# Optimization experiments

Hardware: AMD Instinct MI355X
Metric: run time of the kernel (lower is better)

Reference implementation:

```python
import math
import jax, jax.numpy as jnp
import numpy as np

# h_data constants (init_kwargs)
PITCH = 0.0003      # [m]
FS = 40000000.0     # [Hz]
TX_ANGLE = 0.1      # [rad]
C = 1540.0          # [m/s]
T0 = 0.0            # [s]
CLIP = -70.0        # [dB]
EPS = np.float32(np.finfo(np.float32).eps)


def interplin(v, ds, sq):
    """Vectorized per-column linear interpolation: v(sq[:,k], k).
    v: (N, K) float, sq: (N, K) query points in physical units, ds: step size.
    """
    n = v.shape[0]
    iq = sq / ds
    oob = ~(iq < n - 2)
    iqc = jnp.where(oob, 0.0, iq)
    fl = jnp.floor(iqc).astype(jnp.int32)
    lw = iqc - fl
    v0 = jnp.take_along_axis(v, fl, axis=0)
    v1 = jnp.take_along_axis(v, fl + 1, axis=0)
    vq = v0 * (1.0 - lw) + v1 * lw
    return jnp.where(oob, 0.0, vq)


def fkmig(data):
    """Stolt f-k migration for one (nt, nx) plane-wave RF frame."""
    nt, nx = data.shape
    nt_shift = 2 * math.ceil(T0 * FS / 2)
    nt_fft = 4 * nt + nt_shift              # 8192
    nx_fft = 2 * math.ceil(4 * nx / 2)      # 512
    nf = nt_fft // 2 + 1                    # 4097

    f_vec = jnp.arange(nf, dtype=jnp.float32) * (FS / nt_fft)          # (nf,)
    kx_vec = jnp.roll(jnp.arange(-nx_fft // 2, nx_fft // 2, dtype=jnp.float32) + 1,
                      nx_fft // 2 + 1) / PITCH / nx_fft                # (nx_fft,)
    f = f_vec[:, None]    # (nf, 1)
    kx = kx_vec[None, :]  # (1, nx_fft)

    ol = jnp.fft.fft(data, nt_fft, axis=0)[:nf, :]                     # (nf, nx) complex

    sin_a = math.sin(TX_ANGLE)
    cos_a = math.cos(TX_ANGLE)
    t_delay = sin_a * ((nx - 1) * int(TX_ANGLE < 0)
                       - jnp.arange(nx, dtype=jnp.float32)) * (PITCH / C)  # (nx,)
    ol = ol * jnp.exp(-2j * math.pi * (t_delay + T0)[None, :] * f).astype(jnp.complex64)
    ol = jnp.fft.fft(ol, nx_fft, axis=1)                               # (nf, nx_fft)

    v_erm = C / math.sqrt(1 + cos_a + sin_a ** 2)
    beta = (1 + cos_a) ** 1.5 / (1 + cos_a + sin_a ** 2)
    kz = 2 * f / (beta * C)
    f_kz = v_erm * jnp.sqrt(kx ** 2 + kz ** 2)                         # (nf, nx_fft)

    evanescent = (jnp.abs(f) / (jnp.abs(kx) + EPS)) < C
    ol = jnp.where(evanescent, 0, ol)

    ds = FS / nt_fft
    ol = interplin(ol.real, ds, f_kz) + 1j * interplin(ol.imag, ds, f_kz)
    ol = ol * (f / (f_kz + EPS))
    ol = ol.at[0].set(0)

    # hermitian extension of the half spectrum
    oln = jnp.conj(jnp.fliplr(jnp.roll(ol, -1, axis=1)))
    inv_idx = jnp.arange(nt_fft // 2 - 1, 0, -1)
    ol = jnp.concatenate([ol, oln[inv_idx]], axis=0)                   # (nt_fft, nx_fft)
    ol = jnp.fft.ifft(ol, axis=0)

    gamma = sin_a / (2 - cos_a)
    dx = -gamma * (jnp.arange(nt_fft, dtype=jnp.float32) / FS) * C / 2
    ol = ol * jnp.exp(-2j * math.pi * kx_vec[None, :] * dx[:, None]).astype(jnp.complex64)
    ol = jnp.fft.ifft(ol, axis=1)
    return ol[nt_shift:nt_shift + nt, :nx]                             # (nt, nx) complex


def image_formation(mig):
    """Envelope detection (hilbert along axis 0) + log compression on (nt, nx) real."""
    nt = mig.shape[0]
    Xf = jnp.fft.fft(mig, nt, axis=0)
    h = np.zeros(nt, np.float32)
    if nt % 2 == 0:
        h[0] = h[nt // 2] = 1
        h[1:nt // 2] = 2
    else:
        h[0] = 1
        h[1:(nt + 1) // 2] = 2
    analytic = jnp.fft.ifft(Xf * jnp.asarray(h)[:, None], axis=0)
    img = 20.0 * jnp.log10(jnp.abs(analytic))
    img = img - jnp.max(img)
    img = jnp.where(img < CLIP, CLIP, img)
    return (img + abs(CLIP)) / abs(CLIP)


def setup_inputs() -> dict:
    key = jax.random.key(0)
    data = jax.random.normal(key, (4, 2048, 128), dtype=jnp.float32)
    return {"data": data}


def reference(data):
    mig = jax.vmap(fkmig)(data)                 # (B, nt, nx) complex
    img = jax.vmap(image_formation)(jnp.real(mig))
    return img
```

## Files before the change

kernel.cpp:

```cpp
#include <hip/hip_runtime.h>
#include <cmath>

#define NT 2048
#define NX 128
#define NXF 512
#define NF 4097
#define NFP 4104
#define TDP 2056
#define NBATCH 4
#define EPSF 1.1920929e-07f
#define SOUND_C 1540.0f
#define TWO_PI 6.283185307179586f

__device__ __forceinline__ int SK(int e) { return e + 2 * (e >> 4); }

struct FKP {
  float ds, inv_ds, inv_kx_den, v_erm, kz_coef, ph_rev, dx_coef;
};

__device__ __forceinline__ float2 cmul(float2 a, float2 b) {
  return make_float2(a.x * b.x - a.y * b.y, a.x * b.y + a.y * b.x);
}
__device__ __forceinline__ float2 twid(float u) {
  const float a = u * TWO_PI;
  return make_float2(__cosf(a), __sinf(a));
}
__device__ __forceinline__ float2 twidf(float u) {
  u -= floorf(u);
  return twid(u);
}
__device__ __forceinline__ int dr4_3(unsigned m) {
  unsigned r = __brev(m) >> 26;
  return (int)(((r & 0x15u) << 1) | ((r >> 1) & 0x15u));
}
__device__ __forceinline__ int dr4_4(unsigned m) {
  unsigned r = __brev(m) >> 24;
  return (int)(((r & 0x55u) << 1) | ((r >> 1) & 0x55u));
}
__device__ __forceinline__ int dr4_5(unsigned m) {
  unsigned r = __brev(m) >> 22;
  return (int)(((r & 0x155u) << 1) | ((r >> 1) & 0x155u));
}

__device__ __forceinline__ void dft4(float2& A, float2& B, float2& C, float2& D, float sgn) {
  float2 t0 = make_float2(A.x + C.x, A.y + C.y);
  float2 t1 = make_float2(A.x - C.x, A.y - C.y);
  float2 t2 = make_float2(B.x + D.x, B.y + D.y);
  float2 t3 = make_float2(B.x - D.x, B.y - D.y);
  float2 r  = make_float2(-sgn * t3.y, sgn * t3.x);
  A = make_float2(t0.x + t2.x, t0.y + t2.y);
  B = make_float2(t1.x + r.x, t1.y + r.y);
  C = make_float2(t0.x - t2.x, t0.y - t2.y);
  D = make_float2(t1.x - r.x, t1.y - r.y);
}
__device__ __forceinline__ void bfly4r(float2& A, float2& B, float2& C, float2& D,
                                       float2 w1, float2 w2, float2 w3, float sgn) {
  B = cmul(B, w1); C = cmul(C, w2); D = cmul(D, w3);
  dft4(A, B, C, D, sgn);
}
__device__ __forceinline__ void twtrip(float u, float2& w1, float2& w2, float2& w3) {
  w1 = twid(u); w2 = cmul(w1, w1); w3 = cmul(w2, w1);
}

template<int S>
__device__ __forceinline__ void mstage(float2* __restrict__ s, int base, int kb, float sgn) {
  float2 w[16];
#pragma unroll
  for (int m = 0; m < 16; ++m) w[m] = s[SK(base + S * m)];
  {
    float2 a1, a2, a3; twtrip(sgn * (float)kb * (1.0f / (4 * S)), a1, a2, a3);
#pragma unroll
    for (int a = 0; a < 4; ++a)
      bfly4r(w[4 * a], w[4 * a + 1], w[4 * a + 2], w[4 * a + 3], a1, a2, a3, sgn);
  }
#pragma unroll
  for (int c = 0; c < 4; ++c) {
    float2 b1, b2, b3; twtrip(sgn * (float)(kb + S * c) * (1.0f / (16 * S)), b1, b2, b3);
    bfly4r(w[c], w[4 + c], w[8 + c], w[12 + c], b1, b2, b3, sgn);
  }
#pragma unroll
  for (int m = 0; m < 16; ++m) s[SK(base + S * m)] = w[m];
}

__global__ void __launch_bounds__(256) k_tr(const float* __restrict__ data,
                                            float* __restrict__ dt,
                                            float* __restrict__ red,
                                            size_t slot4, int b_base) {
  __shared__ float tile[32][33];
  if (threadIdx.x == 0 && blockIdx.x == 0 && blockIdx.y == 0)
    *(unsigned*)&red[blockIdx.z * slot4] = 0u;
  const int tx = threadIdx.x & 31;
  const int ty = threadIdx.x >> 5;
  const int t0 = blockIdx.x * 32;
  const int x0 = blockIdx.y * 32;
  const float* In = data + (size_t)(b_base + blockIdx.z) * NT * NX;
  float* Dt = dt + blockIdx.z * slot4;
  for (int i = ty; i < 32; i += 8)
    tile[i][tx] = In[(size_t)(t0 + i) * NX + x0 + tx];
  __syncthreads();
  for (int i = ty; i < 32; i += 8)
    Dt[(size_t)(x0 + i) * TDP + t0 + tx] = tile[tx][i];
}

__global__ void __launch_bounds__(256) k_fft_t(const float* __restrict__ dt,
                                               float2* __restrict__ o1t,
                                               size_t slot4, size_t slot8, FKP P) {
  __shared__ float2 nat[1152];
  __shared__ float2 s[4608];
  const int x = blockIdx.x, tid = threadIdx.x;
  const float2* row2 = (const float2*)(dt + blockIdx.z * slot4 + (size_t)x * TDP);
  float2* O1 = o1t + blockIdx.z * slot8 + (size_t)x * NFP;
  for (int m = tid; m < 1024; m += 256) nat[SK(m)] = row2[m];
  __syncthreads();
  {
    const int m0 = dr4_4((unsigned)tid);
    const float2 v0 = nat[SK(m0)];
    const float2 v1 = nat[SK(m0 + 256)];
    const float2 v2 = nat[SK(m0 + 512)];
    const float2 v3 = nat[SK(m0 + 768)];
    const int base = tid << 4;
#pragma unroll
    for (int k = 0; k < 4; ++k) {
      float2 A = v0, B = v1, C = v2, D = v3;
      if (k == 0) {
        dft4(A, B, C, D, -1.0f);
      } else {
        float2 w1, w2, w3; twtrip(-(float)k * (1.0f / 16.0f), w1, w2, w3);
        bfly4r(A, B, C, D, w1, w2, w3, -1.0f);
      }
      s[SK(base + k)] = A; s[SK(base + 4 + k)] = B;
      s[SK(base + 8 + k)] = C; s[SK(base + 12 + k)] = D;
    }
  }
  __syncthreads();
  mstage<16>(s, ((tid >> 4) << 8) | (tid & 15), tid & 15, -1.0f);
  __syncthreads();
  mstage<256>(s, tid, tid, -1.0f);
  __syncthreads();
  for (int k = tid; k < NF; k += 256) {
    const int ka = k & 4095, kb = (4096 - k) & 4095;
    const float2 Ck = s[SK(ka)];
    const float2 Cm = s[SK(kb)];
    float2 E = make_float2(0.5f * (Ck.x + Cm.x), 0.5f * (Ck.y - Cm.y));
    float2 T = make_float2(0.5f * (Ck.x - Cm.x), 0.5f * (Ck.y + Cm.y));
    float2 WT = cmul(twid((float)k * (-1.0f / 8192.0f)), T);
    float2 X = make_float2(E.x + WT.y, E.y - WT.x);
    float2 ph = twidf(P.ph_rev * (float)(x * k));
    O1[k] = cmul(X, ph);
  }
}

#define R2P 580
__global__ void __launch_bounds__(512) k_fft_x(const float2* __restrict__ o1t,
                                               float2* __restrict__ ot,
                                               size_t slot8, FKP P) {
  __shared__ float2 s[8 * R2P];
  const int i0 = blockIdx.x * 8;
  const int tid = threadIdx.x;
  const float2* O1 = o1t + blockIdx.z * slot8;
  float2* OT = ot + blockIdx.z * slot8;
  for (int idx = tid; idx < 128 * 8; idx += 512) {
    const int ii = idx & 7, x = idx >> 3;
    const int i = i0 + ii;
    float2 v = (i < NF) ? O1[(size_t)x * NFP + i] : make_float2(0.f, 0.f);
    float2* r = s + ii * R2P;
    const int p = ((x & 1) << 8) + 4 * dr4_3((unsigned)(x >> 1));
    r[SK(p)] = v; r[SK(p + 1)] = v; r[SK(p + 2)] = v; r[SK(p + 3)] = v;
  }
  __syncthreads();
  for (int mh = 4; mh <= 64; mh *= 4) {
    const float inv = -1.0f / (float)(4 * mh);
    for (int t = tid; t < 8 * 128; t += 512) {
      const int row = t >> 7, tt = t & 127;
      const int half = tt >> 6, q = tt & 63;
      const int k = q & (mh - 1);
      const int i0b = ((q & ~(mh - 1)) << 2) + k + (half << 8);
      float2* r = s + row * R2P;
      float2 A = r[SK(i0b)], B = r[SK(i0b + mh)], C = r[SK(i0b + 2 * mh)], D = r[SK(i0b + 3 * mh)];
      float2 w1, w2, w3; twtrip((float)k * inv, w1, w2, w3);
      bfly4r(A, B, C, D, w1, w2, w3, -1.0f);
      r[SK(i0b)] = A; r[SK(i0b + mh)] = B; r[SK(i0b + 2 * mh)] = C; r[SK(i0b + 3 * mh)] = D;
    }
    __syncthreads();
  }
  for (int t = tid; t < 8 * 256; t += 512) {
    const int row = t >> 8, k = t & 255;
    float2* r = s + row * R2P;
    float2 E = r[SK(k)], O = r[SK(256 + k)];
    float2 WO = cmul(twid((float)k * (-1.0f / 512.0f)), O);
    r[SK(k)]       = make_float2(E.x + WO.x, E.y + WO.y);
    r[SK(256 + k)] = make_float2(E.x - WO.x, E.y - WO.y);
  }
  __syncthreads();
  for (int idx = tid; idx < 512 * 8; idx += 512) {
    const int j = idx >> 3, ii = idx & 7;
    const int i = i0 + ii;
    if (i >= NF) continue;
    const float f = P.ds * (float)i;
    const int kn = (j <= 256) ? j : j - 512;
    const float kx = fabsf((float)kn * P.inv_kx_den);
    float2 v = (f / (kx + EPSF) < SOUND_C) ? make_float2(0.f, 0.f)
                                           : s[ii * R2P + SK(j)];
    OT[(size_t)j * NFP + i] = v;
  }
}

__global__ void __launch_bounds__(512) k_ifft_t(const float2* __restrict__ ot,
                                                float2* __restrict__ tdt,
                                                size_t slot8, FKP P) {
  __shared__ float2 s[9216];
  const int j = blockIdx.x;
  const int jm = (NXF - j) & (NXF - 1);
  const int t = threadIdx.x;
  const float2* OT = ot + blockIdx.z * slot8;
  float2* T = tdt + blockIdx.z * slot8 + (size_t)j * TDP;
  const float kxj = (float)j * P.inv_kx_den;
  const float kx2 = kxj * kxj;
  const float2* rowj = OT + (size_t)j * NFP;
  const float2* rowm = OT + (size_t)jm * NFP;
  {
    const int tau = t & 255, half = t >> 8;
    const int m0 = dr4_4((unsigned)tau);
    float2 w[16];
#pragma unroll
    for (int m = 0; m < 16; ++m) {
      const int ci = (m & 3) * 1024 + (m >> 2) * 256 + m0;
      const int n = 2 * ci + half;
      const bool mir = (n > 4096);
      const int r = mir ? (8192 - n) : n;
      const float2* rw = mir ? rowm : rowj;
      float2 v = make_float2(0.f, 0.f);
      if (r > 0) {
        const float f = P.ds * (float)r;
        const float kz = f * P.kz_coef;
        const float fkz = P.v_erm * sqrtf(kx2 + kz * kz);
        const float iq = fkz * P.inv_ds;
        if (iq < 4095.0f) {
          const float flf = floorf(iq);
          const int fl = (int)flf;
          const float lw = iq - flf;
          const float2 v0 = rw[fl], v1 = rw[fl + 1];
          const float sc = f / (fkz + EPSF);
          v.x = (v0.x + (v1.x - v0.x) * lw) * sc;
          v.y = (v0.y + (v1.y - v0.y) * lw) * (mir ? -sc : sc);
        }
      }
      w[m] = v;
    }
#pragma unroll
    for (int a = 0; a < 4; ++a) dft4(w[4 * a], w[4 * a + 1], w[4 * a + 2], w[4 * a + 3], 1.0f);
    dft4(w[0], w[4], w[8], w[12], 1.0f);
#pragma unroll
    for (int k = 1; k < 4; ++k) {
      float2 w1, w2, w3; twtrip((float)k * (1.0f / 16.0f), w1, w2, w3);
      bfly4r(w[k], w[4 + k], w[8 + k], w[12 + k], w1, w2, w3, 1.0f);
    }
    const int base = t << 4;
#pragma unroll
    for (int m = 0; m < 16; ++m) s[SK(base + m)] = w[m];
  }
  __syncthreads();
  mstage<16>(s, ((t >> 4) << 8) | (t & 15), t & 15, 1.0f);
  __syncthreads();
  mstage<256>(s, ((t >> 8) << 12) | (t & 255), t & 255, 1.0f);
  __syncthreads();
  const float dxr = -kxj * P.dx_coef;
#pragma unroll
  for (int i = 0; i < 4; ++i) {
    const int k = t + 512 * i;
    const float2 E = s[SK(k)];
    const float2 O = s[SK(4096 + k)];
    const float2 WO = cmul(twid((float)k * (1.0f / 8192.0f)), O);
    const float2 y = make_float2(E.x + WO.x, E.y + WO.y);
    T[k] = cmul(y, twidf(dxr * (float)k));
  }
}

#define SXA 260
#define SXC 292
__global__ void __launch_bounds__(256) k_c2r_x(const float2* __restrict__ tdt,
                                               float* __restrict__ migt,
                                               size_t slot8, size_t slot4) {
  __shared__ float2 sx[8 * SXA];
  __shared__ float2 sc[8 * SXC];
  const int t0 = blockIdx.x * 8;
  const int tid = threadIdx.x;
  const float2* T = tdt + blockIdx.z * slot8;
  float* M = migt + blockIdx.z * slot4;
  for (int idx = tid; idx < 257 * 8; idx += 256) {
    const int tt = idx & 7, jj = idx >> 3;
    float2 v = T[(size_t)jj * TDP + t0 + tt];
    if (jj == 0 || jj == 256) v.y = 0.0f;
    sx[tt * SXA + jj] = v;
  }
  __syncthreads();
  for (int idx = tid; idx < 129 * 8; idx += 256) {
    const int row = idx & 7, k = idx >> 3;
    const float2* X = sx + row * SXA;
    float2* Cb = sc + row * SXC;
    const float2 Xk = X[k];
    const float2 Xm = X[256 - k];
    float2 Ef = make_float2(0.5f * (Xk.x + Xm.x), 0.5f * (Xk.y - Xm.y));
    float2 Tm = make_float2(0.5f * (Xk.x - Xm.x), 0.5f * (Xk.y + Xm.y));
    float2 Of = cmul(twid((float)k * (1.0f / 512.0f)), Tm);
    Cb[SK(dr4_4((unsigned)k))] = make_float2(Ef.x - Of.y, Ef.y + Of.x);
    if (k > 0 && k < 128)
      Cb[SK(dr4_4((unsigned)(256 - k)))] = make_float2(Ef.x + Of.y, Of.x - Ef.y);
  }
  __syncthreads();
  for (int mh = 1; mh <= 64; mh *= 4) {
    const float inv = 1.0f / (float)(4 * mh);
    for (int t = tid; t < 8 * 64; t += 256) {
      const int row = t >> 6, q = t & 63;
      const int k = q & (mh - 1);
      const int i0 = ((q & ~(mh - 1)) << 2) + k;
      float2* r = sc + row * SXC;
      float2 A = r[SK(i0)], B = r[SK(i0 + mh)], C = r[SK(i0 + 2 * mh)], D = r[SK(i0 + 3 * mh)];
      if (mh > 1) {
        float2 w1, w2, w3; twtrip((float)k * inv, w1, w2, w3);
        bfly4r(A, B, C, D, w1, w2, w3, 1.0f);
      } else {
        dft4(A, B, C, D, 1.0f);
      }
      r[SK(i0)] = A; r[SK(i0 + mh)] = B; r[SK(i0 + 2 * mh)] = C; r[SK(i0 + 3 * mh)] = D;
    }
    __syncthreads();
  }
  for (int idx = tid; idx < 128 * 8; idx += 256) {
    const int x = idx >> 3, tt = idx & 7;
    const float2 c = sc[tt * SXC + SK(x >> 1)];
    M[(size_t)x * TDP + t0 + tt] = (x & 1) ? c.y : c.x;
  }
}

__global__ void __launch_bounds__(512) k_hilbert(const float* __restrict__ migt,
                                                 float* __restrict__ migdb,
                                                 float* __restrict__ red,
                                                 size_t slot4) {
  __shared__ float2 s[2304];
  __shared__ float rmax[512];
  const int x = blockIdx.x, tid = threadIdx.x;
  const float* Mr = migt + blockIdx.z * slot4 + (size_t)x * TDP;
  float* Db = migdb + blockIdx.z * slot4 + (size_t)x * TDP;
#pragma unroll
  for (int i = 0; i < 4; ++i) {
    const int p = tid + 512 * i;
    s[SK(p)] = make_float2(Mr[p], 0.0f);
  }
  __syncthreads();
#pragma unroll
  for (int i = 0; i < 2; ++i) {
    const int p = tid + 512 * i;
    const float2 a = s[SK(p)], b = s[SK(p + 1024)];
    s[SK(p)] = make_float2(a.x + b.x, a.y + b.y);
    s[SK(p + 1024)] = cmul(make_float2(a.x - b.x, a.y - b.y),
                           twid(-(float)p * (1.0f / 2048.0f)));
  }
  __syncthreads();
  for (int mh = 256; mh >= 1; mh >>= 2) {
    const int half = tid >> 8, q = tid & 255;
    const int k = q & (mh - 1);
    const int i0 = (half << 10) + ((q & ~(mh - 1)) << 2) + k;
    float2 A = s[SK(i0)], B = s[SK(i0 + mh)], C = s[SK(i0 + 2 * mh)], D = s[SK(i0 + 3 * mh)];
    dft4(A, B, C, D, -1.0f);
    if (mh > 1) {
      float2 w1, w2, w3; twtrip(-(float)k / (float)(4 * mh), w1, w2, w3);
      B = cmul(B, w1); C = cmul(C, w2); D = cmul(D, w3);
    }
    s[SK(i0)] = A; s[SK(i0 + mh)] = B; s[SK(i0 + 2 * mh)] = C; s[SK(i0 + 3 * mh)] = D;
    __syncthreads();
  }
#pragma unroll
  for (int i = 0; i < 4; ++i) {
    const int p = tid + 512 * i;
    const int kk = 2 * dr4_5((unsigned)(p & 1023)) + (p >> 10);
    const float hv = (kk == 0 || kk == 1024) ? 1.0f : ((kk < 1024) ? 2.0f : 0.0f);
    float2 v = s[SK(p)];
    s[SK(p)] = make_float2(v.x * hv, v.y * hv);
  }
  __syncthreads();
  for (int mh = 1; mh <= 256; mh <<= 2) {
    const int half = tid >> 8, q = tid & 255;
    const int k = q & (mh - 1);
    const int i0 = (half << 10) + ((q & ~(mh - 1)) << 2) + k;
    float2 A = s[SK(i0)], B = s[SK(i0 + mh)], C = s[SK(i0 + 2 * mh)], D = s[SK(i0 + 3 * mh)];
    if (mh > 1) {
      float2 w1, w2, w3; twtrip((float)k / (float)(4 * mh), w1, w2, w3);
      bfly4r(A, B, C, D, w1, w2, w3, 1.0f);
    } else {
      dft4(A, B, C, D, 1.0f);
    }
    s[SK(i0)] = A; s[SK(i0 + mh)] = B; s[SK(i0 + 2 * mh)] = C; s[SK(i0 + 3 * mh)] = D;
    __syncthreads();
  }
  float lmax = -3.0e38f;
#pragma unroll
  for (int i = 0; i < 2; ++i) {
    const int p = tid + 512 * i;
    const float2 E = s[SK(p)];
    const float2 O = cmul(s[SK(p + 1024)], twid((float)p * (1.0f / 2048.0f)));
    const float2 y0 = make_float2(E.x + O.x, E.y + O.y);
    const float2 y1 = make_float2(E.x - O.x, E.y - O.y);
    const float d0 = 10.0f * __log10f(fmaxf(y0.x * y0.x + y0.y * y0.y, 1e-30f));
    const float d1 = 10.0f * __log10f(fmaxf(y1.x * y1.x + y1.y * y1.y, 1e-30f));
    Db[p] = d0; Db[p + 1024] = d1;
    lmax = fmaxf(lmax, fmaxf(d0, d1));
  }
  rmax[tid] = lmax;
  __syncthreads();
  for (int w = 256; w > 0; w >>= 1) {
    if (tid < w) rmax[tid] = fmaxf(rmax[tid], rmax[tid + w]);
    __syncthreads();
  }
  if (tid == 0) {
    const unsigned sb = __float_as_uint(rmax[0]);
    const unsigned key = (sb & 0x80000000u) ? ~sb : (sb | 0x80000000u);
    atomicMax((unsigned*)&red[blockIdx.z * slot4], key);
  }
}

__global__ void __launch_bounds__(256) k_norm_tr(const float* __restrict__ migdb,
                                                 const float* __restrict__ red,
                                                 float* __restrict__ out,
                                                 size_t slot4, int b_base) {
  __shared__ float tile[32][33];
  const int tx = threadIdx.x & 31;
  const int ty = threadIdx.x >> 5;
  const int t0 = blockIdx.x * 32;
  const int x0 = blockIdx.y * 32;
  const float* Db = migdb + blockIdx.z * slot4;
  const unsigned kk = *(const unsigned*)&red[blockIdx.z * slot4];
  const float mx = (kk & 0x80000000u) ? __uint_as_float(kk & 0x7FFFFFFFu)
                                      : __uint_as_float(~kk);
  float* O = out + (size_t)(b_base + blockIdx.z) * NT * NX;
  for (int i = ty; i < 32; i += 8)
    tile[i][tx] = Db[(size_t)(x0 + i) * TDP + t0 + tx];
  __syncthreads();
  for (int i = ty; i < 32; i += 8) {
    float v = tile[tx][i] - mx;
    v = fmaxf(v, -70.0f);
    O[(size_t)(t0 + i) * NX + x0 + tx] = (v + 70.0f) * (1.0f / 70.0f);
  }
}

extern "C" void kernel_launch(void* const* d_in, const int* in_sizes, int n_in,
                              void* d_out, int out_size, void* d_ws, size_t ws_size,
                              hipStream_t stream) {
  const float* data = (const float*)d_in[0];
  float* out = (float*)d_out;
  char* ws = (char*)d_ws;

  const size_t O1T_B = 0;
  const size_t OT_B  = (size_t)NX * NFP * sizeof(float2);
  const size_t TDT_B = OT_B + (size_t)NXF * NFP * sizeof(float2);
  const size_t RED_B = TDT_B + (size_t)257 * TDP * sizeof(float2);
  const size_t SLOT_B = ((RED_B + 1024 + 4095) / 4096) * 4096;
  const size_t slot4 = SLOT_B / 4, slot8 = SLOT_B / 8;
  const int slots = (ws_size >= (size_t)NBATCH * SLOT_B) ? NBATCH : 1;

  FKP P;
  {
    const double SA = std::sin(0.1), CA = std::cos(0.1);
    const double A1 = 1.0 + CA + SA * SA;
    const double beta = std::pow(1.0 + CA, 1.5) / A1;
    const double ds = 40000000.0 / 8192.0;
    P.ds = (float)ds;
    P.inv_ds = (float)(8192.0 / 40000000.0);
    P.inv_kx_den = (float)(1.0 / (0.0003 * 512.0));
    P.v_erm = (float)(1540.0 / std::sqrt(A1));
    P.kz_coef = (float)(2.0 / (beta * 1540.0));
    P.ph_rev = (float)(SA * 0.0003 * ds / 1540.0);
    P.dx_coef = (float)(-(SA / (2.0 - CA)) * 1540.0 / (2.0 * 40000000.0));
  }

  float2* o1t  = (float2*)(ws + O1T_B);
  float*  migt = (float*)(ws + O1T_B);
  float2* ot   = (float2*)(ws + OT_B);
  float2* tdt  = (float2*)(ws + TDT_B);
  float*  scr4 = (float*)(ws + TDT_B);
  float*  red  = (float*)(ws + RED_B);

  for (int b0 = 0; b0 < NBATCH; b0 += slots) {
    k_tr     <<<dim3(64, 4, slots), 256, 0, stream>>>(data, scr4, red, slot4, b0);
    k_fft_t  <<<dim3(NX, 1, slots), 256, 0, stream>>>(scr4, o1t, slot4, slot8, P);
    k_fft_x  <<<dim3(513, 1, slots), 512, 0, stream>>>(o1t, ot, slot8, P);
    k_ifft_t <<<dim3(257, 1, slots), 512, 0, stream>>>(ot, tdt, slot8, P);
    k_c2r_x  <<<dim3(256, 1, slots), 256, 0, stream>>>(tdt, migt, slot8, slot4);
    k_hilbert<<<dim3(NX, 1, slots), 512, 0, stream>>>(migt, scr4, red, slot4);
    k_norm_tr<<<dim3(64, 4, slots), 256, 0, stream>>>(scr4, red, out, slot4, b0);
  }
}
```

Before: 158.9 us.

## Restructure x-FFT, batch interpolation loads, and fuse Hilbert stages

k_fft_x now runs with 256 threads. Each thread loads four inputs into registers and performs the first radix-16 stage there, and the final radix-2 combine is merged into the output store, which removes several shared-memory passes and barriers. In k_ifft_t the Stolt interpolation gathers are issued eight at a time without branches, so more memory loads are in flight at once. k_hilbert merges the first radix-2 stage into the load, exploiting the real input, and folds the last forward stage, the Hilbert mask and the first inverse stage into one register pass, dropping two barriers and a full shared-memory sweep.

Measured after the change: 177.2 us. +11.5%, slower.

```diff
diff --git a/kernel.cpp b/kernel.cpp
--- a/kernel.cpp
+++ b/kernel.cpp
@@ -151,7 +151,7 @@
 }
 
 #define R2P 580
-__global__ void __launch_bounds__(512) k_fft_x(const float2* __restrict__ o1t,
+__global__ void __launch_bounds__(256) k_fft_x(const float2* __restrict__ o1t,
                                                float2* __restrict__ ot,
                                                size_t slot8, FKP P) {
   __shared__ float2 s[8 * R2P];
@@ -159,49 +159,51 @@
   const int tid = threadIdx.x;
   const float2* O1 = o1t + blockIdx.z * slot8;
   float2* OT = ot + blockIdx.z * slot8;
-  for (int idx = tid; idx < 128 * 8; idx += 512) {
-    const int ii = idx & 7, x = idx >> 3;
-    const int i = i0 + ii;
-    float2 v = (i < NF) ? O1[(size_t)x * NFP + i] : make_float2(0.f, 0.f);
-    float2* r = s + ii * R2P;
-    const int p = ((x & 1) << 8) + 4 * dr4_3((unsigned)(x >> 1));
-    r[SK(p)] = v; r[SK(p + 1)] = v; r[SK(p + 2)] = v; r[SK(p + 3)] = v;
-  }
-  __syncthreads();
-  for (int mh = 4; mh <= 64; mh *= 4) {
-    const float inv = -1.0f / (float)(4 * mh);
-    for (int t = tid; t < 8 * 128; t += 512) {
-      const int row = t >> 7, tt = t & 127;
-      const int half = tt >> 6, q = tt & 63;
-      const int k = q & (mh - 1);
-      const int i0b = ((q & ~(mh - 1)) << 2) + k + (half << 8);
-      float2* r = s + row * R2P;
-      float2 A = r[SK(i0b)], B = r[SK(i0b + mh)], C = r[SK(i0b + 2 * mh)], D = r[SK(i0b + 3 * mh)];
-      float2 w1, w2, w3; twtrip((float)k * inv, w1, w2, w3);
-      bfly4r(A, B, C, D, w1, w2, w3, -1.0f);
-      r[SK(i0b)] = A; r[SK(i0b + mh)] = B; r[SK(i0b + 2 * mh)] = C; r[SK(i0b + 3 * mh)] = D;
-    }
-    __syncthreads();
-  }
-  for (int t = tid; t < 8 * 256; t += 512) {
-    const int row = t >> 8, k = t & 255;
+  const int row = tid & 7, hu = tid >> 3;
+  const int b = hu & 1, u = hu >> 1;
+  const int i = i0 + row;
+  {
+    float2 v[4];
+#pragma unroll
+    for (int c = 0; c < 4; ++c) {
+      const int m = dr4_3((unsigned)(4 * u + c));
+      const int xx = 2 * m + b;
+      v[c] = (i < NF) ? O1[(size_t)xx * NFP + i] : make_float2(0.f, 0.f);
+    }
     float2* r = s + row * R2P;
-    float2 E = r[SK(k)], O = r[SK(256 + k)];
-    float2 WO = cmul(twid((float)k * (-1.0f / 512.0f)), O);
-    r[SK(k)]       = make_float2(E.x + WO.x, E.y + WO.y);
-    r[SK(256 + k)] = make_float2(E.x - WO.x, E.y - WO.y);
-  }
-  __syncthreads();
-  for (int idx = tid; idx < 512 * 8; idx += 512) {
+    const int base = (b << 8) + (u << 4);
+#pragma unroll
+    for (int k = 0; k < 4; ++k) {
+      float2 A = v[0], B = v[1], C = v[2], D = v[3];
+      if (k == 0) {
+        dft4(A, B, C, D, -1.0f);
+      } else {
+        float2 w1, w2, w3; twtrip(-(float)k * (1.0f / 16.0f), w1, w2, w3);
+        bfly4r(A, B, C, D, w1, w2, w3, -1.0f);
+      }
+      r[SK(base + k)] = A; r[SK(base + 4 + k)] = B;
+      r[SK(base + 8 + k)] = C; r[SK(base + 12 + k)] = D;
+    }
+  }
+  __syncthreads();
+  mstage<16>(s + row * R2P, (b << 8) + u, u, -1.0f);
+  __syncthreads();
+  for (int idx = tid; idx < 512 * 8; idx += 256) {
     const int j = idx >> 3, ii = idx & 7;
-    const int i = i0 + ii;
-    if (i >= NF) continue;
-    const float f = P.ds * (float)i;
+    const int io = i0 + ii;
+    if (io >= NF) continue;
+    const int k = j & 255;
+    const float2* r = s + ii * R2P;
+    const float2 E = r[SK(k)];
+    const float2 O = r[SK(256 + k)];
+    const float2 WO = cmul(twid((float)k * (-1.0f / 512.0f)), O);
+    float2 vv = (j < 256) ? make_float2(E.x + WO.x, E.y + WO.y)
+                          : make_float2(E.x - WO.x, E.y - WO.y);
+    const float f = P.ds * (float)io;
     const int kn = (j <= 256) ? j : j - 512;
     const float kx = fabsf((float)kn * P.inv_kx_den);
-    float2 v = (f / (kx + EPSF) < SOUND_C) ? make_float2(0.f, 0.f)
-                                           : s[ii * R2P + SK(j)];
-    OT[(size_t)j * NFP + i] = v;
+    if (f / (kx + EPSF) < SOUND_C) vv = make_float2(0.f, 0.f);
+    OT[(size_t)j * NFP + io] = vv;
   }
 }
 
@@ -223,29 +225,38 @@
     const int m0 = dr4_4((unsigned)tau);
     float2 w[16];
 #pragma unroll
-    for (int m = 0; m < 16; ++m) {
-      const int ci = (m & 3) * 1024 + (m >> 2) * 256 + m0;
-      const int n = 2 * ci + half;
-      const bool mir = (n > 4096);
-      const int r = mir ? (8192 - n) : n;
-      const float2* rw = mir ? rowm : rowj;
-      float2 v = make_float2(0.f, 0.f);
-      if (r > 0) {
+    for (int g = 0; g < 2; ++g) {
+      float2 v0[8], v1[8];
+      float lw8[8], sc8[8];
+#pragma unroll
+      for (int mm = 0; mm < 8; ++mm) {
+        const int m = g * 8 + mm;
+        const int ci = (m & 3) * 1024 + (m >> 2) * 256 + m0;
+        const int n = 2 * ci + half;
+        const bool mir = (n > 4096);
+        const int r = mir ? (8192 - n) : n;
+        const float2* rw = mir ? rowm : rowj;
         const float f = P.ds * (float)r;
         const float kz = f * P.kz_coef;
         const float fkz = P.v_erm * sqrtf(kx2 + kz * kz);
         const float iq = fkz * P.inv_ds;
-        if (iq < 4095.0f) {
-          const float flf = floorf(iq);
-          const int fl = (int)flf;
-          const float lw = iq - flf;
-          const float2 v0 = rw[fl], v1 = rw[fl + 1];
-          const float sc = f / (fkz + EPSF);
-          v.x = (v0.x + (v1.x - v0.x) * lw) * sc;
-          v.y = (v0.y + (v1.y - v0.y) * lw) * (mir ? -sc : sc);
-        }
+        const bool ok = (r > 0) && (iq < 4095.0f);
+        const float flf = floorf(iq);
+        const int fl = ok ? (int)flf : 0;
+        lw8[mm] = iq - flf;
+        sc8[mm] = ok ? (f / (fkz + EPSF)) : 0.0f;
+        v0[mm] = rw[fl];
+        v1[mm] = rw[fl + 1];
       }
-      w[m] = v;
+#pragma unroll
+      for (int mm = 0; mm < 8; ++mm) {
+        const int m = g * 8 + mm;
+        const int ci = (m & 3) * 1024 + (m >> 2) * 256 + m0;
+        const bool mir = (2 * ci + half > 4096);
+        const float xr = v0[mm].x + (v1[mm].x - v0[mm].x) * lw8[mm];
+        const float yi = v0[mm].y + (v1[mm].y - v0[mm].y) * lw8[mm];
+        w[m] = make_float2(xr * sc8[mm], yi * (mir ? -sc8[mm] : sc8[mm]));
+      }
     }
 #pragma unroll
     for (int a = 0; a < 4; ++a) dft4(w[4 * a], w[4 * a + 1], w[4 * a + 2], w[4 * a + 3], 1.0f);
@@ -343,53 +354,50 @@
   const float* Mr = migt + blockIdx.z * slot4 + (size_t)x * TDP;
   float* Db = migdb + blockIdx.z * slot4 + (size_t)x * TDP;
 #pragma unroll
-  for (int i = 0; i < 4; ++i) {
-    const int p = tid + 512 * i;
-    s[SK(p)] = make_float2(Mr[p], 0.0f);
-  }
-  __syncthreads();
-#pragma unroll
   for (int i = 0; i < 2; ++i) {
     const int p = tid + 512 * i;
-    const float2 a = s[SK(p)], b = s[SK(p + 1024)];
-    s[SK(p)] = make_float2(a.x + b.x, a.y + b.y);
-    s[SK(p + 1024)] = cmul(make_float2(a.x - b.x, a.y - b.y),
-                           twid(-(float)p * (1.0f / 2048.0f)));
-  }
-  __syncthreads();
-  for (int mh = 256; mh >= 1; mh >>= 2) {
+    const float a = Mr[p], b = Mr[p + 1024];
+    s[SK(p)] = make_float2(a + b, 0.0f);
+    const float2 wv = twid(-(float)p * (1.0f / 2048.0f));
+    s[SK(p + 1024)] = make_float2((a - b) * wv.x, (a - b) * wv.y);
+  }
+  __syncthreads();
+  for (int mh = 256; mh >= 4; mh >>= 2) {
     const int half = tid >> 8, q = tid & 255;
     const int k = q & (mh - 1);
     const int i0 = (half << 10) + ((q & ~(mh - 1)) << 2) + k;
     float2 A = s[SK(i0)], B = s[SK(i0 + mh)], C = s[SK(i0 + 2 * mh)], D = s[SK(i0 + 3 * mh)];
     dft4(A, B, C, D, -1.0f);
-    if (mh > 1) {
+    {
       float2 w1, w2, w3; twtrip(-(float)k / (float)(4 * mh), w1, w2, w3);
       B = cmul(B, w1); C = cmul(C, w2); D = cmul(D, w3);
     }
     s[SK(i0)] = A; s[SK(i0 + mh)] = B; s[SK(i0 + 2 * mh)] = C; s[SK(i0 + 3 * mh)] = D;
     __syncthreads();
   }
-#pragma unroll
-  for (int i = 0; i < 4; ++i) {
-    const int p = tid + 512 * i;
-    const int kk = 2 * dr4_5((unsigned)(p & 1023)) + (p >> 10);
-    const float hv = (kk == 0 || kk == 1024) ? 1.0f : ((kk < 1024) ? 2.0f : 0.0f);
-    float2 v = s[SK(p)];
-    s[SK(p)] = make_float2(v.x * hv, v.y * hv);
-  }
-  __syncthreads();
-  for (int mh = 1; mh <= 256; mh <<= 2) {
+  {
+    const int half = tid >> 8, q = tid & 255;
+    const int i0 = (half << 10) + (q << 2);
+    float2 A = s[SK(i0)], B = s[SK(i0 + 1)], C = s[SK(i0 + 2)], D = s[SK(i0 + 3)];
+    dft4(A, B, C, D, -1.0f);
+    const int r = 2 * dr4_4((unsigned)q) + half;
+    const float h0 = (r == 0) ? 1.0f : 2.0f;
+    const float h2 = (r == 0) ? 1.0f : 0.0f;
+    A.x *= h0; A.y *= h0;
+    B.x *= 2.0f; B.y *= 2.0f;
+    C.x *= h2; C.y *= h2;
+    D = make_float2(0.0f, 0.0f);
+    dft4(A, B, C, D, 1.0f);
+    s[SK(i0)] = A; s[SK(i0 + 1)] = B; s[SK(i0 + 2)] = C; s[SK(i0 + 3)] = D;
+  }
+  __syncthreads();
+  for (int mh = 4; mh <= 256; mh <<= 2) {
     const int half = tid >> 8, q = tid & 255;
     const int k = q & (mh - 1);
     const int i0 = (half << 10) + ((q & ~(mh - 1)) << 2) + k;
     float2 A = s[SK(i0)], B = s[SK(i0 + mh)], C = s[SK(i0 + 2 * mh)], D = s[SK(i0 + 3 * mh)];
-    if (mh > 1) {
-      float2 w1, w2, w3; twtrip((float)k / (float)(4 * mh), w1, w2, w3);
-      bfly4r(A, B, C, D, w1, w2, w3, 1.0f);
-    } else {
-      dft4(A, B, C, D, 1.0f);
-    }
+    float2 w1, w2, w3; twtrip((float)k / (float)(4 * mh), w1, w2, w3);
+    bfly4r(A, B, C, D, w1, w2, w3, 1.0f);
     s[SK(i0)] = A; s[SK(i0 + mh)] = B; s[SK(i0 + 2 * mh)] = C; s[SK(i0 + 3 * mh)] = D;
     __syncthreads();
   }
@@ -483,7 +491,7 @@
   for (int b0 = 0; b0 < NBATCH; b0 += slots) {
     k_tr     <<<dim3(64, 4, slots), 256, 0, stream>>>(data, scr4, red, slot4, b0);
     k_fft_t  <<<dim3(NX, 1, slots), 256, 0, stream>>>(scr4, o1t, slot4, slot8, P);
-    k_fft_x  <<<dim3(513, 1, slots), 512, 0, stream>>>(o1t, ot, slot8, P);
+    k_fft_x  <<<dim3(513, 1, slots), 256, 0, stream>>>(o1t, ot, slot8, P);
     k_ifft_t <<<dim3(257, 1, slots), 512, 0, stream>>>(ot, tdt, slot8, P);
     k_c2r_x  <<<dim3(256, 1, slots), 256, 0, stream>>>(tdt, migt, slot8, slot4);
     k_hilbert<<<dim3(NX, 1, slots), 512, 0, stream>>>(migt, scr4, red, slot4);
```
